# Optimization experiments

Hardware: AMD Instinct MI355X
Metric: run time of the kernel (lower is better)

The kernel has to match this reference:

```python
import jax, jax.numpy as jnp
import numpy as np

DIMS, HEAD, FREQ = 1024, 16, 10000
HEAD_DIM = DIMS // HEAD          # 64
ROT = HEAD_DIM // 2              # 32
B, S = 4, 8192


def setup_inputs() -> dict:
    key = jax.random.key(0)
    k1, k2, k3, k4 = jax.random.split(key, 4)
    x = jax.random.normal(k1, (B, S, DIMS), dtype=jnp.float32)
    matrix = jax.random.normal(k2, (HEAD_DIM, HEAD_DIM), dtype=jnp.float32)
    thetas = jax.random.normal(k3, (ROT,), dtype=jnp.float32) * 0.1
    tscale = jnp.ones((1,), dtype=jnp.float32)
    # inverse frequencies exactly as in __init__
    invf = (1.0 / FREQ ** (jnp.arange(0, HEAD_DIM, 2, dtype=jnp.float32) / HEAD_DIM)).astype(jnp.float32)
    pairs = jax.random.randint(k4, (ROT, 2), 0, HEAD_DIM, dtype=jnp.int32)
    return {"x": x, "matrix": matrix, "thetas": thetas, "tscale": tscale,
            "invf": invf, "pairs": pairs}


def _composed_rotation(thetas, tscale, pairs, d, dtype):
    # Build every Givens matrix G_k (same element-set order as the torch code)
    theta = thetas * tscale[0]

    def make_G(i, j, th):
        c, sn = jnp.cos(th), jnp.sin(th)
        G = jnp.eye(d, dtype=dtype)
        return G.at[i, i].set(c).at[j, j].set(c).at[i, j].set(-sn).at[j, i].set(sn)

    Gs = jax.vmap(make_G)(pairs[:, 0], pairs[:, 1], theta)  # [rot, d, d]

    def step(acc, G):
        return acc @ G, None

    G_comb, _ = jax.lax.scan(step, jnp.eye(d, dtype=dtype), Gs)
    return G_comb


def reference(x, matrix, thetas, tscale, invf, pairs):
    b, s, dims = x.shape
    d = matrix.shape[0]          # head_dim
    h = dims // d                # heads

    G_comb = _composed_rotation(thetas, tscale, pairs, d, x.dtype)

    xr = x.reshape(b, s, h, d)
    # flat @ G_combined @ self.matrix (acts on last dim)
    xr = xr @ (G_comb @ matrix)

    # sinusoidal RoPE: sinusoid[s, d/2] = pos * invf
    pos = jnp.arange(s, dtype=x.dtype)
    sinusoid = pos[:, None] * invf[None, :]
    sin = jnp.sin(sinusoid)[None, :, None, :]   # [1, s, 1, d/2]
    cos = jnp.cos(sinusoid)[None, :, None, :]

    x1, x2 = xr[..., ::2], xr[..., 1::2]
    out = jnp.concatenate([x1 * cos - x2 * sin, x1 * sin + x2 * cos], axis=-1)
    return out.reshape(b, s, dims) * jnp.asarray(np.sqrt(dims), x.dtype)
```

## Files before the change

kernel.cpp:

```cpp
#include <hip/hip_runtime.h>
#include <math.h>

#define BB 4
#define SS 8192
#define HH 16
#define DD 64
#define ROT 32
#define NG (BB * SS * HH)
#define RPT 64
#define TILES 4
#define NBLK (NG / (RPT * TILES))
#define TPB 256
#define OSTR 65
#define LSTR 65

typedef float f32x4 __attribute__((ext_vector_type(4)));
typedef short bf16x8 __attribute__((ext_vector_type(8)));

__global__ void setup_GM(const float* __restrict__ thetas,
                         const float* __restrict__ tscale,
                         const int* __restrict__ pairs,
                         const float* __restrict__ matrix,
                         float* __restrict__ M,
                         unsigned short* __restrict__ Mhi,
                         unsigned short* __restrict__ Mlo) {
  __shared__ float Gs[DD][DD];
  const int t = threadIdx.x;
  if (t < DD) {
    for (int c = 0; c < DD; ++c) Gs[t][c] = (t == c) ? 1.0f : 0.0f;
    const float ts = tscale[0];
    for (int r = 0; r < ROT; ++r) {
      const int i = pairs[2 * r], j = pairs[2 * r + 1];
      const float th = thetas[r] * ts;
      const float cc = cosf(th), sn = sinf(th);
      if (i == j) {
        Gs[t][i] *= sn;
      } else {
        const float a = Gs[t][i], b = Gs[t][j];
        Gs[t][i] = a * cc + b * sn;
        Gs[t][j] = b * cc - a * sn;
      }
    }
  }
  __syncthreads();
  const int e = blockIdx.x * 256 + t;
  const int k = e >> 6, col = e & 63;
  float a0 = 0.f, a1 = 0.f, a2 = 0.f, a3 = 0.f;
  for (int kk = 0; kk < DD; kk += 4) {
    a0 = fmaf(Gs[k][kk], matrix[kk * DD + col], a0);
    a1 = fmaf(Gs[k][kk + 1], matrix[(kk + 1) * DD + col], a1);
    a2 = fmaf(Gs[k][kk + 2], matrix[(kk + 2) * DD + col], a2);
    a3 = fmaf(Gs[k][kk + 3], matrix[(kk + 3) * DD + col], a3);
  }
  const float val = (a0 + a1) + (a2 + a3);
  M[e] = val;

  const int K2 = k >> 5, T = col >> 4;
  const int lane = ((k >> 3) & 3) * 16 + (col & 15);
  const int idx = ((T * 2 + K2) * 64 + lane) * 8 + (k & 7);
  const unsigned int b = __float_as_uint(val);
  const unsigned int hb = b & 0xFFFF0000u;
  const float rem = val - __uint_as_float(hb);
  Mhi[idx] = (unsigned short)(b >> 16);
  Mlo[idx] = (unsigned short)(__float_as_uint(rem) >> 16);
}

__global__ void setup_table(const float* __restrict__ invf,
                            float* __restrict__ tab) {
  const int idx = blockIdx.x * 256 + threadIdx.x;
  if (idx >= SS * 32) return;
  const int s = idx >> 5, d = idx & 31;
  const float ang = (float)s * invf[d];
  tab[s * 64 + d] = 32.0f * cosf(ang);
  tab[s * 64 + 32 + d] = 32.0f * sinf(ang);
}

__device__ __forceinline__ unsigned int pack_hi(float u, float v, float& ru,
                                                float& rv) {
  const unsigned int bu = __float_as_uint(u);
  const unsigned int bv = __float_as_uint(v);
  const unsigned int hv = bv & 0xFFFF0000u;
  ru = u - __uint_as_float(bu & 0xFFFF0000u);
  rv = v - __uint_as_float(hv);
  return (bu >> 16) | hv;
}
__device__ __forceinline__ unsigned int pack_lo(float ru, float rv) {
  return (__float_as_uint(ru) >> 16) | (__float_as_uint(rv) & 0xFFFF0000u);
}
__device__ __forceinline__ void cvt8(const f32x4 a, const f32x4 b, bf16x8& hi,
                                     bf16x8& lo) {
  unsigned int* hp = (unsigned int*)&hi;
  unsigned int* lp = (unsigned int*)&lo;
  float r0, r1;
  hp[0] = pack_hi(a[0], a[1], r0, r1);
  lp[0] = pack_lo(r0, r1);
  hp[1] = pack_hi(a[2], a[3], r0, r1);
  lp[1] = pack_lo(r0, r1);
  hp[2] = pack_hi(b[0], b[1], r0, r1);
  lp[2] = pack_lo(r0, r1);
  hp[3] = pack_hi(b[2], b[3], r0, r1);
  lp[3] = pack_lo(r0, r1);
}

__global__ __launch_bounds__(TPB, 2) void apply_rot(
    const float* __restrict__ x, const unsigned short* __restrict__ Mhi,
    const unsigned short* __restrict__ Mlo, const float* __restrict__ tab,
    float* __restrict__ out) {
  __shared__ float po[4 * 16 * OSTR];
  const int tid = threadIdx.x;
  const int w = tid >> 6;
  const int l = tid & 63;
  const int l15 = l & 15, lk = l >> 4;
  const int odd = l & 1;
  const int dloc = l15 >> 1;

  bf16x8 bh[8], bl[8];
#pragma unroll
  for (int f = 0; f < 8; ++f) {
    bh[f] = *(const bf16x8*)(Mhi + (f * 64 + l) * 8);
    bl[f] = *(const bf16x8*)(Mlo + (f * 64 + l) * 8);
  }

  const size_t R0 = (size_t)blockIdx.x * (RPT * TILES);
  const float* __restrict__ xp = x + (R0 + w * 16 + l15) * DD + lk * 8;
  float* __restrict__ pw = po + w * 16 * OSTR;

  f32x4 x0 = *(const f32x4*)(xp);
  f32x4 x1 = *(const f32x4*)(xp + 4);
  f32x4 x2 = *(const f32x4*)(xp + 32);
  f32x4 x3 = *(const f32x4*)(xp + 36);

#pragma unroll 1
  for (int t = 0; t < TILES; ++t) {
    bf16x8 ah0, al0, ah1, al1;
    cvt8(x0, x1, ah0, al0);
    cvt8(x2, x3, ah1, al1);

    if (t + 1 < TILES) {
      xp += RPT * DD;
      x0 = *(const f32x4*)(xp);
      x1 = *(const f32x4*)(xp + 4);
      x2 = *(const f32x4*)(xp + 32);
      x3 = *(const f32x4*)(xp + 36);
    }

    f32x4 acc[4];
#pragma unroll
    for (int T = 0; T < 4; ++T) {
      f32x4 a = {0.f, 0.f, 0.f, 0.f};
      a = __builtin_amdgcn_mfma_f32_16x16x32_bf16(ah0, bh[T * 2 + 0], a, 0, 0, 0);
      a = __builtin_amdgcn_mfma_f32_16x16x32_bf16(ah1, bh[T * 2 + 1], a, 0, 0, 0);
      a = __builtin_amdgcn_mfma_f32_16x16x32_bf16(ah0, bl[T * 2 + 0], a, 0, 0, 0);
      a = __builtin_amdgcn_mfma_f32_16x16x32_bf16(ah1, bl[T * 2 + 1], a, 0, 0, 0);
      a = __builtin_amdgcn_mfma_f32_16x16x32_bf16(al0, bh[T * 2 + 0], a, 0, 0, 0);
      a = __builtin_amdgcn_mfma_f32_16x16x32_bf16(al1, bh[T * 2 + 1], a, 0, 0, 0);
      acc[T] = a;
    }

    const int spos = (int)((R0 >> 4) + t * 4 + w) & (SS - 1);
    const float* __restrict__ tb = tab + spos * 64;
#pragma unroll
    for (int T = 0; T < 4; ++T) {
      const float cz = tb[8 * T + dloc];
      const float sz = tb[32 + 8 * T + dloc];
      const int ocol = (odd ? 32 : 0) + 8 * T + dloc;
#pragma unroll
      for (int q = 0; q < 4; ++q) {
        const float v = acc[T][q];
        const float p = __shfl_xor(v, 1);
        const float ps = p * sz;
        const float res = fmaf(v, cz, odd ? ps : -ps);
        pw[(lk * 4 + q) * OSTR + ocol] = res;
      }
    }

    float* __restrict__ og = out + (R0 + (size_t)t * RPT + w * 16) * DD;
#pragma unroll
    for (int jj = 0; jj < 4; ++jj) {
      const int f = jj * 64 + l;
      const int row = f >> 4, c4 = (f & 15) * 4;
      const f32x4 v = *(const f32x4*)&pw[row * OSTR + c4];
      __builtin_nontemporal_store(v, (f32x4*)(og + row * DD + c4));
    }
  }
}

__global__ __launch_bounds__(256, 8) void apply_rot_fb(
    const float* __restrict__ x, const float* __restrict__ M,
    const float* __restrict__ invf, float* __restrict__ out) {
  __shared__ float lds[64 * LSTR];
  const int tid = threadIdx.x;
  const size_t R0 = (size_t)blockIdx.x * 64;
  const float4* __restrict__ xg = (const float4*)x + R0 * 16;
#pragma unroll
  for (int i = 0; i < 4; ++i) {
    const int f = i * 256 + tid;
    *(float4*)&lds[(f >> 4) * LSTR + (f & 15) * 4] = xg[f];
  }
  __syncthreads();
  const int r = tid & 63;
  const int h = __builtin_amdgcn_readfirstlane(tid >> 6);
  const float* __restrict__ Mh = M + h * 16;
  const float* __restrict__ xr = &lds[r * LSTR];
  float acc[16];
#pragma unroll
  for (int c = 0; c < 16; ++c) acc[c] = 0.0f;
#pragma unroll 4
  for (int k4 = 0; k4 < 16; ++k4) {
    const float4 xv = *(const float4*)&xr[k4 * 4];
    const float* __restrict__ m0 = Mh + k4 * 4 * DD;
#pragma unroll
    for (int c = 0; c < 16; ++c) acc[c] = fmaf(xv.x, m0[c], acc[c]);
#pragma unroll
    for (int c = 0; c < 16; ++c) acc[c] = fmaf(xv.y, m0[DD + c], acc[c]);
#pragma unroll
    for (int c = 0; c < 16; ++c) acc[c] = fmaf(xv.z, m0[2 * DD + c], acc[c]);
#pragma unroll
    for (int c = 0; c < 16; ++c) acc[c] = fmaf(xv.w, m0[3 * DD + c], acc[c]);
  }
  const int g = (int)R0 + r;
  const int spos = (g >> 4) & (SS - 1);
  float cz[8], sz[8];
#pragma unroll
  for (int d = 0; d < 8; ++d) {
    const float ang = (float)spos * invf[h * 8 + d];
    cz[d] = 32.0f * cosf(ang);
    sz[d] = 32.0f * sinf(ang);
  }
  float4 lov[2], hiv[2];
#pragma unroll
  for (int q = 0; q < 2; ++q) {
#pragma unroll
    for (int d = 0; d < 4; ++d) {
      const int dd = 4 * q + d;
      const float e = acc[2 * dd], o = acc[2 * dd + 1];
      ((float*)&lov[q])[d] = e * cz[dd] - o * sz[dd];
      ((float*)&hiv[q])[d] = e * sz[dd] + o * cz[dd];
    }
  }
  __syncthreads();
  float* __restrict__ orow = &lds[r * LSTR];
  *(float4*)&orow[8 * h + 0] = lov[0];
  *(float4*)&orow[8 * h + 4] = lov[1];
  *(float4*)&orow[32 + 8 * h + 0] = hiv[0];
  *(float4*)&orow[32 + 8 * h + 4] = hiv[1];
  __syncthreads();
  float4* __restrict__ og = (float4*)out + R0 * 16;
#pragma unroll
  for (int i = 0; i < 4; ++i) {
    const int f = i * 256 + tid;
    og[f] = *(float4*)&lds[(f >> 4) * LSTR + (f & 15) * 4];
  }
}

extern "C" void kernel_launch(void* const* d_in, const int* in_sizes, int n_in,
                              void* d_out, int out_size, void* d_ws,
                              size_t ws_size, hipStream_t stream) {
  const float* x = (const float*)d_in[0];
  const float* matrix = (const float*)d_in[1];
  const float* thetas = (const float*)d_in[2];
  const float* tscale = (const float*)d_in[3];
  const float* invf = (const float*)d_in[4];
  const int* pairs = (const int*)d_in[5];
  float* out = (float*)d_out;

  float* M = (float*)d_ws;
  unsigned short* Mhi = (unsigned short*)(M + DD * DD);
  unsigned short* Mlo = Mhi + DD * DD;
  float* tab = (float*)(Mlo + DD * DD);
  const size_t need =
      (size_t)DD * DD * 4 + (size_t)DD * DD * 4 + (size_t)SS * 64 * 4;
  const bool have_tab = ws_size >= need;

  setup_GM<<<16, 256, 0, stream>>>(thetas, tscale, pairs, matrix, M, Mhi, Mlo);
  if (have_tab) {
    setup_table<<<(SS * 32) / 256, 256, 0, stream>>>(invf, tab);
    apply_rot<<<NBLK, TPB, 0, stream>>>(x, Mhi, Mlo, tab, out);
  } else {
    apply_rot_fb<<<NG / 64, 256, 0, stream>>>(x, M, invf, out);
  }
}
```

Before: 263.2 us.

## Permute matrix columns so RoPE pairs land in-lane, drop LDS staging, deepen prefetch

Reorders the packed bf16 matrix columns so even and odd rotary partners fall in separate MFMA accumulator tiles within the same lane. The RoPE combine then needs no cross-lane shuffle and no shared-memory transpose, and results are stored straight to global memory. The cos/sin table is repacked so each lane fetches one float4. Input prefetch is deepened to two tiles ahead and the occupancy hint is raised to 3. The trade-off is that output stores become scalar, 4-byte and strided instead of coalesced 16-byte vectors, and register pressure rises.

```diff
diff --git a/kernel.cpp b/kernel.cpp
--- a/kernel.cpp
+++ b/kernel.cpp
@@ -11,7 +11,6 @@
 #define TILES 4
 #define NBLK (NG / (RPT * TILES))
 #define TPB 256
-#define OSTR 65
 #define LSTR 65
 
 typedef float f32x4 __attribute__((ext_vector_type(4)));
@@ -55,9 +54,11 @@
   const float val = (a0 + a1) + (a2 + a3);
   M[e] = val;
 
-  const int K2 = k >> 5, T = col >> 4;
-  const int lane = ((k >> 3) & 3) * 16 + (col & 15);
-  const int idx = ((T * 2 + K2) * 64 + lane) * 8 + (k & 7);
+  const int G = ((col >> 5) << 1) | (col & 1);
+  const int v = (col >> 1) & 15;
+  const int lane = ((k >> 3) & 3) * 16 + v;
+  const int f = G * 2 + (k >> 5);
+  const int idx = (f * 64 + lane) * 8 + (k & 7);
   const unsigned int b = __float_as_uint(val);
   const unsigned int hb = b & 0xFFFF0000u;
   const float rem = val - __uint_as_float(hb);
@@ -65,14 +66,19 @@
   Mlo[idx] = (unsigned short)(__float_as_uint(rem) >> 16);
 }
 
-__global__ void setup_table(const float* __restrict__ invf,
-                            float* __restrict__ tab) {
+__global__ void setup_tab2(const float* __restrict__ invf,
+                           float* __restrict__ tab2) {
   const int idx = blockIdx.x * 256 + threadIdx.x;
-  if (idx >= SS * 32) return;
-  const int s = idx >> 5, d = idx & 31;
-  const float ang = (float)s * invf[d];
-  tab[s * 64 + d] = 32.0f * cosf(ang);
-  tab[s * 64 + 32 + d] = 32.0f * sinf(ang);
+  if (idx >= SS * 16) return;
+  const int s = idx >> 4, i = idx & 15;
+  const float a0 = (float)s * invf[i];
+  const float a1 = (float)s * invf[16 + i];
+  float4 v;
+  v.x = 32.0f * cosf(a0);
+  v.y = 32.0f * sinf(a0);
+  v.z = 32.0f * cosf(a1);
+  v.w = 32.0f * sinf(a1);
+  ((float4*)tab2)[idx] = v;
 }
 
 __device__ __forceinline__ unsigned int pack_hi(float u, float v, float& ru,
@@ -102,17 +108,14 @@
   lp[3] = pack_lo(r0, r1);
 }
 
-__global__ __launch_bounds__(TPB, 2) void apply_rot(
+__global__ __launch_bounds__(TPB, 3) void apply_rot(
     const float* __restrict__ x, const unsigned short* __restrict__ Mhi,
-    const unsigned short* __restrict__ Mlo, const float* __restrict__ tab,
+    const unsigned short* __restrict__ Mlo, const float* __restrict__ tab2,
     float* __restrict__ out) {
-  __shared__ float po[4 * 16 * OSTR];
   const int tid = threadIdx.x;
   const int w = tid >> 6;
   const int l = tid & 63;
   const int l15 = l & 15, lk = l >> 4;
-  const int odd = l & 1;
-  const int dloc = l15 >> 1;
 
   bf16x8 bh[8], bl[8];
 #pragma unroll
@@ -123,66 +126,73 @@
 
   const size_t R0 = (size_t)blockIdx.x * (RPT * TILES);
   const float* __restrict__ xp = x + (R0 + w * 16 + l15) * DD + lk * 8;
-  float* __restrict__ pw = po + w * 16 * OSTR;
-
-  f32x4 x0 = *(const f32x4*)(xp);
-  f32x4 x1 = *(const f32x4*)(xp + 4);
-  f32x4 x2 = *(const f32x4*)(xp + 32);
-  f32x4 x3 = *(const f32x4*)(xp + 36);
+  float* __restrict__ ob = out + (R0 + w * 16) * DD;
+  const int tok0 = (int)(R0 >> 4) + w;
+
+  f32x4 a0 = *(const f32x4*)(xp);
+  f32x4 a1 = *(const f32x4*)(xp + 4);
+  f32x4 a2 = *(const f32x4*)(xp + 32);
+  f32x4 a3 = *(const f32x4*)(xp + 36);
+  const float* __restrict__ xq = xp + (size_t)RPT * DD;
+  f32x4 b0 = *(const f32x4*)(xq);
+  f32x4 b1 = *(const f32x4*)(xq + 4);
+  f32x4 b2 = *(const f32x4*)(xq + 32);
+  f32x4 b3 = *(const f32x4*)(xq + 36);
+
+#define PROC(C0, C1, C2, C3, T)                                              \
+  {                                                                          \
+    bf16x8 ah0, al0, ah1, al1;                                               \
+    cvt8(C0, C1, ah0, al0);                                                  \
+    cvt8(C2, C3, ah1, al1);                                                  \
+    if ((T) + 2 < TILES) {          \
+      const float* __restrict__ p = xp + (size_t)((T) + 2) * RPT * DD;       \
+      C0 = *(const f32x4*)(p);                                               \
+      C1 = *(const f32x4*)(p + 4);                                           \
+      C2 = *(const f32x4*)(p + 32);                                          \
+      C3 = *(const f32x4*)(p + 36);                                          \
+    }                                                                        \
+    const int spos = (tok0 + (T) * 4) & (SS - 1);                            \
+    const f32x4 tv = *(const f32x4*)(tab2 + (size_t)spos * 64 + l15 * 4);    \
+    f32x4 acc[4];                                                            \
+    _Pragma("unroll") for (int G = 0; G < 4; ++G) {                          \
+      f32x4 a_ = {0.f, 0.f, 0.f, 0.f};                                       \
+      a_ = __builtin_amdgcn_mfma_f32_16x16x32_bf16(ah0, bh[2 * G], a_, 0, 0, \
+                                                   0);                       \
+      a_ = __builtin_amdgcn_mfma_f32_16x16x32_bf16(ah1, bh[2 * G + 1], a_,   \
+                                                   0, 0, 0);                 \
+      a_ = __builtin_amdgcn_mfma_f32_16x16x32_bf16(ah0, bl[2 * G], a_, 0, 0, \
+                                                   0);                       \
+      a_ = __builtin_amdgcn_mfma_f32_16x16x32_bf16(ah1, bl[2 * G + 1], a_,   \
+                                                   0, 0, 0);                 \
+      a_ = __builtin_amdgcn_mfma_f32_16x16x32_bf16(al0, bh[2 * G], a_, 0, 0, \
+                                                   0);                       \
+      a_ = __builtin_amdgcn_mfma_f32_16x16x32_bf16(al1, bh[2 * G + 1], a_,   \
+                                                   0, 0, 0);                 \
+      acc[G] = a_;                                                           \
+    }                                                                        \
+    float* __restrict__ og = ob + (size_t)(T)*RPT * DD;                      \
+    _Pragma("unroll") for (int g = 0; g < 2; ++g) {                          \
+      const f32x4 ae = acc[2 * g];              \
+      const f32x4 ao = acc[2 * g + 1];          \
+      const float cz = tv[2 * g], sz = tv[2 * g + 1];                        \
+      float* __restrict__ ogg = og + g * 16 + l15;                           \
+      _Pragma("unroll") for (int q = 0; q < 4; ++q) {                        \
+        const float e_ = ae[q], o_ = ao[q];                                  \
+        const float lo_ = fmaf(e_, cz, -(o_ * sz));                          \
+        const float hi_ = fmaf(e_, sz, o_ * cz);                             \
+        const int ro = (lk * 4 + q) * DD;                                    \
+        __builtin_nontemporal_store(lo_, ogg + ro);                          \
+        __builtin_nontemporal_store(hi_, ogg + ro + 32);                     \
+      }                                                                      \
+    }                                                                        \
+  }
 
 #pragma unroll 1
-  for (int t = 0; t < TILES; ++t) {
-    bf16x8 ah0, al0, ah1, al1;
-    cvt8(x0, x1, ah0, al0);
-    cvt8(x2, x3, ah1, al1);
-
-    if (t + 1 < TILES) {
-      xp += RPT * DD;
-      x0 = *(const f32x4*)(xp);
-      x1 = *(const f32x4*)(xp + 4);
-      x2 = *(const f32x4*)(xp + 32);
-      x3 = *(const f32x4*)(xp + 36);
-    }
-
-    f32x4 acc[4];
-#pragma unroll
-    for (int T = 0; T < 4; ++T) {
-      f32x4 a = {0.f, 0.f, 0.f, 0.f};
-      a = __builtin_amdgcn_mfma_f32_16x16x32_bf16(ah0, bh[T * 2 + 0], a, 0, 0, 0);
-      a = __builtin_amdgcn_mfma_f32_16x16x32_bf16(ah1, bh[T * 2 + 1], a, 0, 0, 0);
-      a = __builtin_amdgcn_mfma_f32_16x16x32_bf16(ah0, bl[T * 2 + 0], a, 0, 0, 0);
-      a = __builtin_amdgcn_mfma_f32_16x16x32_bf16(ah1, bl[T * 2 + 1], a, 0, 0, 0);
-      a = __builtin_amdgcn_mfma_f32_16x16x32_bf16(al0, bh[T * 2 + 0], a, 0, 0, 0);
-      a = __builtin_amdgcn_mfma_f32_16x16x32_bf16(al1, bh[T * 2 + 1], a, 0, 0, 0);
-      acc[T] = a;
-    }
-
-    const int spos = (int)((R0 >> 4) + t * 4 + w) & (SS - 1);
-    const float* __restrict__ tb = tab + spos * 64;
-#pragma unroll
-    for (int T = 0; T < 4; ++T) {
-      const float cz = tb[8 * T + dloc];
-      const float sz = tb[32 + 8 * T + dloc];
-      const int ocol = (odd ? 32 : 0) + 8 * T + dloc;
-#pragma unroll
-      for (int q = 0; q < 4; ++q) {
-        const float v = acc[T][q];
-        const float p = __shfl_xor(v, 1);
-        const float ps = p * sz;
-        const float res = fmaf(v, cz, odd ? ps : -ps);
-        pw[(lk * 4 + q) * OSTR + ocol] = res;
-      }
-    }
-
-    float* __restrict__ og = out + (R0 + (size_t)t * RPT + w * 16) * DD;
-#pragma unroll
-    for (int jj = 0; jj < 4; ++jj) {
-      const int f = jj * 64 + l;
-      const int row = f >> 4, c4 = (f & 15) * 4;
-      const f32x4 v = *(const f32x4*)&pw[row * OSTR + c4];
-      __builtin_nontemporal_store(v, (f32x4*)(og + row * DD + c4));
-    }
-  }
+  for (int t = 0; t < TILES; t += 2) {
+    PROC(a0, a1, a2, a3, t);
+    PROC(b0, b1, b2, b3, t + 1);
+  }
+#undef PROC
 }
 
 __global__ __launch_bounds__(256, 8) void apply_rot_fb(
@@ -267,15 +277,15 @@
   float* M = (float*)d_ws;
   unsigned short* Mhi = (unsigned short*)(M + DD * DD);
   unsigned short* Mlo = Mhi + DD * DD;
-  float* tab = (float*)(Mlo + DD * DD);
+  float* tab2 = (float*)(Mlo + DD * DD);
   const size_t need =
       (size_t)DD * DD * 4 + (size_t)DD * DD * 4 + (size_t)SS * 64 * 4;
   const bool have_tab = ws_size >= need;
 
   setup_GM<<<16, 256, 0, stream>>>(thetas, tscale, pairs, matrix, M, Mhi, Mlo);
   if (have_tab) {
-    setup_table<<<(SS * 32) / 256, 256, 0, stream>>>(invf, tab);
-    apply_rot<<<NBLK, TPB, 0, stream>>>(x, Mhi, Mlo, tab, out);
+    setup_tab2<<<(SS * 16) / 256, 256, 0, stream>>>(invf, tab2);
+    apply_rot<<<NBLK, TPB, 0, stream>>>(x, Mhi, Mlo, tab2, out);
   } else {
     apply_rot_fb<<<NG / 64, 256, 0, stream>>>(x, M, invf, out);
   }
```

New measurement: 272.6 us. +3.6%, slower.
